# Performance work log

Measured on AMD Instinct MI355X. Metric: run time of the kernel, lower is better.

Reference implementation:

```python
import jax, jax.numpy as jnp
import numpy as np
from jax import lax


def conv2d_same(x, w):
    # x: [N,C,H,W], w: [O,I,3,3] -> [N,O,H,W], stride 1, padding 1
    return lax.conv_general_dilated(x, w, (1, 1), 'SAME',
                                    dimension_numbers=('NCHW', 'OIHW', 'NCHW'))


def bilinear_gather(x, py, px):
    # x: [N,C,H,W]; py,px: [N,K,H,W] float sampling coords (zero pad outside)
    # returns [N,C,K,H,W]
    N, C, H, W = x.shape
    y0f = jnp.floor(py)
    x0f = jnp.floor(px)
    wy = (py - y0f)[:, None]  # [N,1,K,H,W]
    wx = (px - x0f)[:, None]
    y0 = y0f.astype(jnp.int32)
    x0 = x0f.astype(jnp.int32)
    flat = x.reshape(N, C, H * W)

    def gather(yi, xi):
        valid = ((yi >= 0) & (yi < H) & (xi >= 0) & (xi < W))
        yc = jnp.clip(yi, 0, H - 1)
        xc = jnp.clip(xi, 0, W - 1)
        idx = (yc * W + xc).reshape(N, 1, -1)          # [N,1,K*H*W]
        g = jnp.take_along_axis(flat, jnp.broadcast_to(idx, (N, C, idx.shape[-1])), axis=2)
        g = g.reshape(N, C, *yi.shape[1:])             # [N,C,K,H,W]
        return g * valid.astype(x.dtype)[:, None]

    v00 = gather(y0, x0)
    v01 = gather(y0, x0 + 1)
    v10 = gather(y0 + 1, x0)
    v11 = gather(y0 + 1, x0 + 1)
    return (v00 * (1 - wy) * (1 - wx) + v01 * (1 - wy) * wx
            + v10 * wy * (1 - wx) + v11 * wy * wx)


def deform_conv(x, off, w, b):
    # x: [N,C,H,W]; off: [N,18,H,W] (dy,dx per 3x3 tap); w: [O,C,3,3]; b: [O]
    N, C, H, W = x.shape
    K = 9
    off = off.reshape(N, K, 2, H, W)
    kdy, kdx = jnp.meshgrid(jnp.arange(3) - 1, jnp.arange(3) - 1, indexing='ij')
    kdy = kdy.reshape(K).astype(x.dtype)
    kdx = kdx.reshape(K).astype(x.dtype)
    hh = jnp.arange(H, dtype=x.dtype)
    ww = jnp.arange(W, dtype=x.dtype)
    py = off[:, :, 0] + hh[None, None, :, None] + kdy[None, :, None, None]  # [N,K,H,W]
    px = off[:, :, 1] + ww[None, None, None, :] + kdx[None, :, None, None]
    sampled = bilinear_gather(x, py, px)               # [N,C,K,H,W]
    out = jnp.einsum('nckhw,ock->nohw', sampled, w.reshape(w.shape[0], C, K))
    return out + b[None, :, None, None]


def setup_inputs() -> dict:
    key = jax.random.key(0)
    ks = jax.random.split(key, 8)
    B, obj, C, H, W = 2, 4, 256, 48, 48
    return {
        'query': jax.random.normal(ks[0], (B, C, H, W), jnp.float32),
        'key': jax.random.normal(ks[1], (B, C, H, W), jnp.float32),
        'value': jax.random.normal(ks[2], (B, obj, C, H, W), jnp.float32),
        'off_conv_w': jax.random.normal(ks[3], (C, 2 * C, 3, 3), jnp.float32) * 0.02,
        'off_conv_b': jnp.zeros((C,), jnp.float32),
        'offp_w': jax.random.normal(ks[4], (18, C, 3, 3), jnp.float32) * 0.02,
        'offp_b': jnp.zeros((18,), jnp.float32),
        'deform_w': jax.random.normal(ks[5], (C, C, 3, 3), jnp.float32) * 0.02,
        'deform_b': jnp.zeros((C,), jnp.float32),
    }


def reference(query, key, value, off_conv_w, off_conv_b, offp_w, offp_b, deform_w, deform_b):
    B, obj, C, H, W = value.shape
    N = B * obj
    concat = jnp.concatenate([query, key], axis=1)                    # [B,2C,H,W]
    feat = conv2d_same(concat, off_conv_w) + off_conv_b[None, :, None, None]
    feat = jnp.broadcast_to(feat[:, None], (B, obj, C, H, W)).reshape(N, C, H, W)
    x = value.reshape(N, C, H, W)
    off = conv2d_same(feat, offp_w) + offp_b[None, :, None, None]     # [N,18,H,W]
    out = deform_conv(x, off, deform_w, deform_b)                     # [N,C,H,W]
    out = out.reshape(N, C, H * W).transpose(2, 0, 1)                 # [HW,N,C]
    q = jnp.broadcast_to(query[:, None], (B, obj, C, H, W)).reshape(N, C, H * W)
    return q.transpose(2, 0, 1) + out
```

## Files before the change

kernel.cpp:

```cpp
#include <hip/hip_runtime.h>

#define HH 48
#define WW 48
#define HWP 2304
#define CC 256
#define NB 8
#define QKROW 2305

typedef __attribute__((ext_vector_type(8))) short short8;
typedef __attribute__((ext_vector_type(4))) short bf16x4;
typedef __attribute__((ext_vector_type(4))) float floatx4;

static __device__ __forceinline__ unsigned short f2bf(float f) {
    union { float f; unsigned u; } v; v.f = f;
    unsigned r = v.u + 0x7fffu + ((v.u >> 16) & 1u);
    return (unsigned short)(r >> 16);
}
static __device__ __forceinline__ float bf2f(short v) {
    union { unsigned u; float f; } x; x.u = ((unsigned)(unsigned short)v) << 16;
    return x.f;
}

__global__ __launch_bounds__(256) void k_tr(const float* __restrict__ q,
        const float* __restrict__ kk, const float* __restrict__ v,
        unsigned short* __restrict__ qkT, float* __restrict__ qT,
        unsigned short* __restrict__ vT) {
    __shared__ float T[64][65];
    const int pg = blockIdx.x, cg = blockIdx.y, z = blockIdx.z;
    const int tx = threadIdx.x & 63, ty = threadIdx.x >> 6;
    if (z < 4) {
        const int b = z >> 1, src = z & 1;
        const float* s = (src ? kk : q) + (size_t)b * CC * HWP;
#pragma unroll
        for (int i = 0; i < 16; i++) {
            int cl = ty * 16 + i;
            T[cl][tx] = s[(size_t)(cg * 64 + cl) * HWP + pg * 64 + tx];
        }
        __syncthreads();
#pragma unroll
        for (int i = 0; i < 16; i++) {
            int pxl = ty * 16 + i;
            float val = T[tx][pxl];
            qkT[((size_t)b * QKROW + pg * 64 + pxl) * 512 + src * 256 + cg * 64 + tx]
                = f2bf(val);
            if (src == 0)
                qT[((size_t)(pg * 64 + pxl) * 2 + b) * 256 + cg * 64 + tx] = val;
        }
    } else {
        const int n = z - 4;
        const float* s = v + (size_t)n * CC * HWP;
#pragma unroll
        for (int i = 0; i < 16; i++) {
            int cl = ty * 16 + i;
            T[cl][tx] = s[(size_t)(cg * 64 + cl) * HWP + pg * 64 + tx];
        }
        __syncthreads();
#pragma unroll
        for (int i = 0; i < 16; i++) {
            int pxl = ty * 16 + i;
            vT[((size_t)n * HWP + pg * 64 + pxl) * 256 + cg * 64 + tx] = f2bf(T[tx][pxl]);
        }
    }
}

__global__ __launch_bounds__(256) void k_prep_w(const float* __restrict__ w1,
        const float* __restrict__ dw, const float* __restrict__ w2,
        unsigned short* __restrict__ w1r, unsigned short* __restrict__ wdr,
        unsigned short* __restrict__ w2r, unsigned short* __restrict__ qkT,
        unsigned short* __restrict__ featb) {
    if (blockIdx.x == 7200) {
        int t = threadIdx.x;
#pragma unroll
        for (int b = 0; b < 2; b++) {
            qkT[((size_t)b * QKROW + HWP) * 512 + t] = 0;
            qkT[((size_t)b * QKROW + HWP) * 512 + 256 + t] = 0;
            featb[((size_t)b * QKROW + HWP) * 256 + t] = 0;
        }
        return;
    }
    int idx = blockIdx.x * 256 + threadIdx.x;
    if (idx < 1179648) {
        int j = idx & 7, l = (idx >> 3) & 63, mtg = (idx >> 9) & 15;
        int kk = (idx >> 13) & 15, tap = idx >> 17;
        int o = mtg * 16 + (l & 15);
        int c2 = kk * 32 + (l >> 4) * 8 + j;
        w1r[idx] = f2bf(w1[((size_t)o * 512 + c2) * 9 + tap]);
    } else if (idx < 1179648 + 589824) {
        int i2 = idx - 1179648;
        int j = i2 & 7, l = (i2 >> 3) & 63, mtg = (i2 >> 9) & 15;
        int kk = (i2 >> 13) & 7, tap = i2 >> 16;
        int o = mtg * 16 + (l & 15);
        int c = kk * 32 + (l >> 4) * 8 + j;
        wdr[i2] = f2bf(dw[((size_t)o * 256 + c) * 9 + tap]);
    } else {
        int i2 = idx - 1179648 - 589824;
        int j = i2 & 7, l = (i2 >> 3) & 63, mt = (i2 >> 9) & 1;
        int kk = (i2 >> 10) & 7, tap = i2 >> 13;
        int o = mt * 16 + (l & 15);
        int c = kk * 32 + (l >> 4) * 8 + j;
        w2r[i2] = (o < 18) ? f2bf(w2[((size_t)o * 256 + c) * 9 + tap]) : 0;
    }
}

__global__ __launch_bounds__(512, 4) void k_conv1(const unsigned short* __restrict__ qkT,
        const unsigned short* __restrict__ w1r, const float* __restrict__ b1,
        unsigned short* __restrict__ featb) {
    __shared__ __align__(16) unsigned short Bl[2][32 * 64 * 8];

    const int tid = threadIdx.x;
    const int pt = blockIdx.x;
    const int b  = blockIdx.y;
    const int oh = blockIdx.z;
    const int px0 = pt * 32;
    const int lane = tid & 63, wv = tid >> 6;
    const int lo = lane & 15, quad = lane >> 4;
    const int mtg = oh * 8 + wv;

    floatx4 acc[2];
    acc[0] = (floatx4)0.f; acc[1] = (floatx4)0.f;

    short8 R[4];
    auto stage_load = [&](int tap) {
        const int dy = tap / 3 - 1, dx = tap % 3 - 1;
#pragma unroll
        for (int k = 0; k < 4; k++) {
            int seg = tid + k * 512;
            int cl  = seg >> 6;
            int sl  = seg & 63;
            int px  = px0 + cl;
            int h = px / WW, w = px - (px / WW) * WW;
            bool val = (h + dy >= 0) && (h + dy < HH)
                       && (w + dx >= 0) && (w + dx < WW);
            int row = val ? (px + dy * WW + dx) : HWP;
            R[k] = *(const short8*)(qkT + ((size_t)b * QKROW + row) * 512 + sl * 8);
        }
    };

    stage_load(0);
    int buf = 0;

    for (int tap = 0; tap < 9; tap++) {
        unsigned short* sb = &Bl[buf][0];
#pragma unroll
        for (int k = 0; k < 4; k++) {
            int seg = tid + k * 512;
            int cl = seg >> 6, sl = seg & 63;
            int slw = sl ^ (cl & 7);
            *(short8*)(sb + ((size_t)cl * 64 + slw) * 8) = R[k];
        }
        __syncthreads();

        if (tap < 8) stage_load(tap + 1);

        const unsigned short* afr = w1r + (((size_t)tap * 16 * 16 + mtg) * 64 + lane) * 8;
#pragma unroll 4
        for (int ks = 0; ks < 16; ks++) {
            short8 a = *(const short8*)(afr + (size_t)ks * 16 * 512);
#pragma unroll
            for (int nt = 0; nt < 2; nt++) {
                int cl = nt * 16 + lo;
                int slot = (ks * 4 + quad) ^ (cl & 7);
                short8 bf = *(const short8*)(sb + ((size_t)cl * 64 + slot) * 8);
                acc[nt] = __builtin_amdgcn_mfma_f32_16x16x32_bf16(a, bf, acc[nt], 0, 0, 0);
            }
        }
        buf ^= 1;
    }

    const int o = mtg * 16 + quad * 4;
    const float b0 = b1[o], bb1 = b1[o + 1], bb2 = b1[o + 2], bb3 = b1[o + 3];
#pragma unroll
    for (int nt = 0; nt < 2; nt++) {
        int px = px0 + nt * 16 + lo;
        bf16x4 pk;
        pk[0] = (short)f2bf(acc[nt][0] + b0);
        pk[1] = (short)f2bf(acc[nt][1] + bb1);
        pk[2] = (short)f2bf(acc[nt][2] + bb2);
        pk[3] = (short)f2bf(acc[nt][3] + bb3);
        *(bf16x4*)(featb + ((size_t)b * QKROW + px) * 256 + o) = pk;
    }
}

__global__ __launch_bounds__(256) void k_conv2(const unsigned short* __restrict__ featb,
        const unsigned short* __restrict__ w2r, float* __restrict__ off9) {
    const int tid = threadIdx.x;
    const int pb = blockIdx.x;
    const int b  = blockIdx.y;
    const int tap = blockIdx.z;
    const int lane = tid & 63, wv = tid >> 6;
    const int lo = lane & 15, quad = lane >> 4;
    const int pp = pb * 64 + wv * 16 + lo;
    const int h = pp / WW, w = pp - (pp / WW) * WW;
    const int dy = tap / 3 - 1, dx = tap % 3 - 1;
    const bool val = (h + dy >= 0) && (h + dy < HH) && (w + dx >= 0) && (w + dx < WW);
    const int row = val ? (pp + dy * WW + dx) : HWP;

    const unsigned short* brow = featb + ((size_t)b * QKROW + row) * 256 + quad * 8;
    const unsigned short* afr = w2r + (((size_t)tap * 8 * 2) * 64 + lane) * 8;

    floatx4 acc[2];
    acc[0] = (floatx4)0.f; acc[1] = (floatx4)0.f;
#pragma unroll
    for (int ks = 0; ks < 8; ks++) {
        short8 bf = *(const short8*)(brow + ks * 32);
        const unsigned short* ak = afr + (size_t)ks * 2 * 512;
        short8 a0 = *(const short8*)(ak);
        short8 a1 = *(const short8*)(ak + 512);
        acc[0] = __builtin_amdgcn_mfma_f32_16x16x32_bf16(a0, bf, acc[0], 0, 0, 0);
        acc[1] = __builtin_amdgcn_mfma_f32_16x16x32_bf16(a1, bf, acc[1], 0, 0, 0);
    }

    float* dst = off9 + (((size_t)tap * 2 + b) * HWP + pp) * 32;
#pragma unroll
    for (int mt = 0; mt < 2; mt++) {
        int o = mt * 16 + quad * 4;
        *(floatx4*)(dst + o) = acc[mt];
    }
}

__global__ __launch_bounds__(256) void k_osum(const float* __restrict__ off9,
        const float* __restrict__ b2, float* __restrict__ off) {
    int i = blockIdx.x * 256 + threadIdx.x;
    int b = i / (18 * HWP);
    int r = i - b * 18 * HWP;
    int o = r / HWP, px = r - o * HWP;
    float s = b2[o];
#pragma unroll
    for (int t = 0; t < 9; t++)
        s += off9[(((size_t)t * 2 + b) * HWP + px) * 32 + o];
    off[i] = s;
}

__global__ __launch_bounds__(512, 2) void k_deform(const unsigned short* __restrict__ vT,
        const float* __restrict__ off, const unsigned short* __restrict__ wdr,
        const float* __restrict__ db, const float* __restrict__ qT,
        float* __restrict__ out) {
    __shared__ __align__(16) unsigned short Sl[2][80 * 256];

    const int tid = threadIdx.x;
    const int bid = blockIdx.x;
    const int c0 = (((bid & 7) << 5) + (bid >> 3)) * 72;
    const int lane = tid & 63, wv = tid >> 6;
    const int lo = lane & 15, quad = lane >> 4;
    const int colg = tid >> 5;
    const int slice = tid & 31;

    int u_pq[5];
    float u_m[5];
    const float* u_off[5];
    const unsigned short* u_vT[5];
#pragma unroll
    for (int u = 0; u < 5; u++) {
        int cl = colg + u * 16;
        int cg = min(c0 + cl, 18431);
        int pq = cg >> 3, n = cg & 7;
        u_pq[u] = pq;
        u_m[u]  = (cl < 72) ? 1.f : 0.f;
        u_off[u] = off + (size_t)(n >> 2) * 18 * HWP + pq;
        u_vT[u]  = vT + (size_t)n * HWP * 256 + slice * 8;
    }

    floatx4 acc[2][5];
#pragma unroll
    for (int mt = 0; mt < 2; mt++)
#pragma unroll
        for (int nt = 0; nt < 5; nt++) acc[mt][nt] = (floatx4)0.f;

    short8 P[5][4];
    float  cwt[5][4];
    float  ndy[5], ndx[5];

    auto prefetch_off = [&](int tap) {
#pragma unroll
        for (int u = 0; u < 5; u++) {
            ndy[u] = u_off[u][(2 * tap) * HWP];
            ndx[u] = u_off[u][(2 * tap + 1) * HWP];
        }
    };

    auto prefetch_body = [&](int tap) {
        const float kdy = (float)(tap / 3 - 1), kdx = (float)(tap % 3 - 1);
#pragma unroll
        for (int u = 0; u < 5; u++) {
            int pq = u_pq[u];
            int h = pq / WW, w = pq - (pq / WW) * WW;
            float py = ndy[u] + (float)h + kdy;
            float px = ndx[u] + (float)w + kdx;
            float y0f = floorf(py), x0f = floorf(px);
            int y0 = (int)y0f, x0 = (int)x0f;
            float fy = py - y0f, fx = px - x0f;
            bool y0ok = (y0 >= 0) & (y0 < HH), y1ok = (y0 >= -1) & (y0 < HH - 1);
            bool x0ok = (x0 >= 0) & (x0 < WW), x1ok = (x0 >= -1) & (x0 < WW - 1);
            int y0c = min(max(y0, 0), HH - 1), y1c = min(max(y0 + 1, 0), HH - 1);
            int x0c = min(max(x0, 0), WW - 1), x1c = min(max(x0 + 1, 0), WW - 1);
            const unsigned short* r0 = u_vT[u] + (size_t)(y0c * WW + x0c) * 256;
            const unsigned short* r1 = u_vT[u] + (size_t)(y0c * WW + x1c) * 256;
            const unsigned short* r2 = u_vT[u] + (size_t)(y1c * WW + x0c) * 256;
            const unsigned short* r3 = u_vT[u] + (size_t)(y1c * WW + x1c) * 256;
            float m = u_m[u];
            cwt[u][0] = (y0ok && x0ok) ? m * (1.f - fy) * (1.f - fx) : 0.f;
            cwt[u][1] = (y0ok && x1ok) ? m * (1.f - fy) * fx         : 0.f;
            cwt[u][2] = (y1ok && x0ok) ? m * fy * (1.f - fx)         : 0.f;
            cwt[u][3] = (y1ok && x1ok) ? m * fy * fx                 : 0.f;
            P[u][0] = *(const short8*)(r0);
            P[u][1] = *(const short8*)(r1);
            P[u][2] = *(const short8*)(r2);
            P[u][3] = *(const short8*)(r3);
        }
    };

    prefetch_off(0);
    prefetch_body(0);
    int buf = 0;

    for (int tap = 0; tap < 9; tap++) {
        if (tap < 8) prefetch_off(tap + 1);
        unsigned short* sb = &Sl[buf][0];
#pragma unroll
        for (int u = 0; u < 5; u++) {
            float w0 = cwt[u][0], w1 = cwt[u][1], w2 = cwt[u][2], w3 = cwt[u][3];
            short8 ov;
#pragma unroll
            for (int j = 0; j < 8; j++) {
                float s = w0 * bf2f(P[u][0][j]) + w1 * bf2f(P[u][1][j])
                        + w2 * bf2f(P[u][2][j]) + w3 * bf2f(P[u][3][j]);
                ov[j] = (short)f2bf(s);
            }
            int cl = colg + u * 16;
            int slot = slice ^ (cl & 7);
            *(short8*)(sb + cl * 256 + slot * 8) = ov;
        }
        __syncthreads();

        if (tap < 8) prefetch_body(tap + 1);

        const unsigned short* afr = wdr + (((size_t)tap * 8 * 16 + wv * 2) * 64 + lane) * 8;
#pragma unroll
        for (int ks = 0; ks < 8; ks++) {
            const unsigned short* ak = afr + (size_t)ks * 16 * 512;
            short8 a0 = *(const short8*)(ak);
            short8 a1 = *(const short8*)(ak + 512);
#pragma unroll
            for (int nt = 0; nt < 5; nt++) {
                int cl = nt * 16 + lo;
                int slot = (ks * 4 + quad) ^ (cl & 7);
                short8 bf = *(const short8*)(sb + cl * 256 + slot * 8);
                acc[0][nt] = __builtin_amdgcn_mfma_f32_16x16x32_bf16(a0, bf, acc[0][nt], 0, 0, 0);
                acc[1][nt] = __builtin_amdgcn_mfma_f32_16x16x32_bf16(a1, bf, acc[1][nt], 0, 0, 0);
            }
        }
        __syncthreads();
        buf ^= 1;
    }

#pragma unroll
    for (int mt = 0; mt < 2; mt++) {
        int o = wv * 32 + mt * 16 + quad * 4;
        float d0 = db[o], d1 = db[o + 1], d2 = db[o + 2], d3 = db[o + 3];
#pragma unroll
        for (int nt = 0; nt < 5; nt++) {
            int cl = nt * 16 + lo;
            if (cl < 72) {
                int cg = c0 + cl;
                int pq = cg >> 3, b = (cg & 7) >> 2;
                floatx4 qv = *(const floatx4*)(qT + ((size_t)pq * 2 + b) * 256 + o);
                floatx4 r = acc[mt][nt];
                r[0] += d0 + qv[0];
                r[1] += d1 + qv[1];
                r[2] += d2 + qv[2];
                r[3] += d3 + qv[3];
                *(floatx4*)(out + (size_t)cg * CC + o) = r;
            }
        }
    }
}

extern "C" void kernel_launch(void* const* d_in, const int* in_sizes, int n_in,
                              void* d_out, int out_size, void* d_ws, size_t ws_size,
                              hipStream_t stream) {
    const float* q  = (const float*)d_in[0];
    const float* k  = (const float*)d_in[1];
    const float* v  = (const float*)d_in[2];
    const float* w1 = (const float*)d_in[3];
    const float* b1 = (const float*)d_in[4];
    const float* w2 = (const float*)d_in[5];
    const float* b2 = (const float*)d_in[6];
    const float* dw = (const float*)d_in[7];
    const float* db = (const float*)d_in[8];
    float* out = (float*)d_out;

    float* off   = (float*)d_ws;
    float* qT    = off + 82944;
    float* off9  = qT + 3538944;
    unsigned short* qkT   = (unsigned short*)(off9 + 1327104);
    unsigned short* vT    = qkT + 2360320;
    unsigned short* featb = vT + 4718592;
    unsigned short* w1r   = featb + 1180160;
    unsigned short* wdr   = w1r + 1179648;
    unsigned short* w2r   = wdr + 589824;

    hipLaunchKernelGGL(k_tr,    dim3(36, 4, 12), dim3(256), 0, stream, q, k, v, qkT, qT, vT);
    hipLaunchKernelGGL(k_prep_w,dim3(7201),      dim3(256), 0, stream, w1, dw, w2, w1r, wdr, w2r, qkT, featb);
    hipLaunchKernelGGL(k_conv1, dim3(72, 2, 2),  dim3(512), 0, stream, qkT, w1r, b1, featb);
    hipLaunchKernelGGL(k_conv2, dim3(36, 2, 9),  dim3(256), 0, stream, featb, w2r, off9);
    hipLaunchKernelGGL(k_osum,  dim3(324),       dim3(256), 0, stream, off9, b2, off);
    hipLaunchKernelGGL(k_deform,dim3(256),       dim3(512), 0, stream, vT, off, wdr, db, qT, out);
}
```

Measured before the change: 207.3 us.

## Merge transpose and weight-prep kernels; fuse tap reduction into offset conv

Combines the input transpose and weight reorder kernels into one launch with a flattened block index. Rewrites the offset conv so each block loops over all nine taps, staging shifted feature rows through double-buffered, swizzled shared memory and accumulating in registers. It then adds the bias and writes final offsets directly, removing the per-tap partial buffer and the separate summation kernel. This saves two launches and the partial-sum memory round-trip, but the conv now runs only 72 blocks, which reduces parallelism.

```diff
diff --git a/kernel.cpp b/kernel.cpp
--- a/kernel.cpp
+++ b/kernel.cpp
@@ -21,12 +21,54 @@
     return x.f;
 }
 
-__global__ __launch_bounds__(256) void k_tr(const float* __restrict__ q,
+__global__ __launch_bounds__(256) void k_trprep(const float* __restrict__ q,
         const float* __restrict__ kk, const float* __restrict__ v,
-        unsigned short* __restrict__ qkT, float* __restrict__ qT,
-        unsigned short* __restrict__ vT) {
+        const float* __restrict__ w1, const float* __restrict__ dw,
+        const float* __restrict__ w2, unsigned short* __restrict__ qkT,
+        float* __restrict__ qT, unsigned short* __restrict__ vT,
+        unsigned short* __restrict__ w1r, unsigned short* __restrict__ wdr,
+        unsigned short* __restrict__ w2r, unsigned short* __restrict__ featb) {
     __shared__ float T[64][65];
-    const int pg = blockIdx.x, cg = blockIdx.y, z = blockIdx.z;
+    const int bid = blockIdx.x;
+    if (bid < 7201) {
+        if (bid == 7200) {
+            int t = threadIdx.x;
+#pragma unroll
+            for (int b = 0; b < 2; b++) {
+                qkT[((size_t)b * QKROW + HWP) * 512 + t] = 0;
+                qkT[((size_t)b * QKROW + HWP) * 512 + 256 + t] = 0;
+                featb[((size_t)b * QKROW + HWP) * 256 + t] = 0;
+            }
+            return;
+        }
+        int idx = bid * 256 + threadIdx.x;
+        if (idx < 1179648) {
+            int j = idx & 7, l = (idx >> 3) & 63, mtg = (idx >> 9) & 15;
+            int kkk = (idx >> 13) & 15, tap = idx >> 17;
+            int o = mtg * 16 + (l & 15);
+            int c2 = kkk * 32 + (l >> 4) * 8 + j;
+            w1r[idx] = f2bf(w1[((size_t)o * 512 + c2) * 9 + tap]);
+        } else if (idx < 1179648 + 589824) {
+            int i2 = idx - 1179648;
+            int j = i2 & 7, l = (i2 >> 3) & 63, mtg = (i2 >> 9) & 15;
+            int kkk = (i2 >> 13) & 7, tap = i2 >> 16;
+            int o = mtg * 16 + (l & 15);
+            int c = kkk * 32 + (l >> 4) * 8 + j;
+            wdr[i2] = f2bf(dw[((size_t)o * 256 + c) * 9 + tap]);
+        } else {
+            int i2 = idx - 1179648 - 589824;
+            int j = i2 & 7, l = (i2 >> 3) & 63, mt = (i2 >> 9) & 1;
+            int kkk = (i2 >> 10) & 7, tap = i2 >> 13;
+            int o = mt * 16 + (l & 15);
+            int c = kkk * 32 + (l >> 4) * 8 + j;
+            w2r[i2] = (o < 18) ? f2bf(w2[((size_t)o * 256 + c) * 9 + tap]) : 0;
+        }
+        return;
+    }
+    const int idx2 = bid - 7201;
+    const int pg = idx2 % 36;
+    const int rest = idx2 / 36;
+    const int cg = rest & 3, z = rest >> 2;
     const int tx = threadIdx.x & 63, ty = threadIdx.x >> 6;
     if (z < 4) {
         const int b = z >> 1, src = z & 1;
@@ -60,45 +102,6 @@
             int pxl = ty * 16 + i;
             vT[((size_t)n * HWP + pg * 64 + pxl) * 256 + cg * 64 + tx] = f2bf(T[tx][pxl]);
         }
-    }
-}
-
-__global__ __launch_bounds__(256) void k_prep_w(const float* __restrict__ w1,
-        const float* __restrict__ dw, const float* __restrict__ w2,
-        unsigned short* __restrict__ w1r, unsigned short* __restrict__ wdr,
-        unsigned short* __restrict__ w2r, unsigned short* __restrict__ qkT,
-        unsigned short* __restrict__ featb) {
-    if (blockIdx.x == 7200) {
-        int t = threadIdx.x;
-#pragma unroll
-        for (int b = 0; b < 2; b++) {
-            qkT[((size_t)b * QKROW + HWP) * 512 + t] = 0;
-            qkT[((size_t)b * QKROW + HWP) * 512 + 256 + t] = 0;
-            featb[((size_t)b * QKROW + HWP) * 256 + t] = 0;
-        }
-        return;
-    }
-    int idx = blockIdx.x * 256 + threadIdx.x;
-    if (idx < 1179648) {
-        int j = idx & 7, l = (idx >> 3) & 63, mtg = (idx >> 9) & 15;
-        int kk = (idx >> 13) & 15, tap = idx >> 17;
-        int o = mtg * 16 + (l & 15);
-        int c2 = kk * 32 + (l >> 4) * 8 + j;
-        w1r[idx] = f2bf(w1[((size_t)o * 512 + c2) * 9 + tap]);
-    } else if (idx < 1179648 + 589824) {
-        int i2 = idx - 1179648;
-        int j = i2 & 7, l = (i2 >> 3) & 63, mtg = (i2 >> 9) & 15;
-        int kk = (i2 >> 13) & 7, tap = i2 >> 16;
-        int o = mtg * 16 + (l & 15);
-        int c = kk * 32 + (l >> 4) * 8 + j;
-        wdr[i2] = f2bf(dw[((size_t)o * 256 + c) * 9 + tap]);
-    } else {
-        int i2 = idx - 1179648 - 589824;
-        int j = i2 & 7, l = (i2 >> 3) & 63, mt = (i2 >> 9) & 1;
-        int kk = (i2 >> 10) & 7, tap = i2 >> 13;
-        int o = mt * 16 + (l & 15);
-        int c = kk * 32 + (l >> 4) * 8 + j;
-        w2r[i2] = (o < 18) ? f2bf(w2[((size_t)o * 256 + c) * 9 + tap]) : 0;
     }
 }
 
@@ -181,54 +184,74 @@
     }
 }
 
-__global__ __launch_bounds__(256) void k_conv2(const unsigned short* __restrict__ featb,
-        const unsigned short* __restrict__ w2r, float* __restrict__ off9) {
+__global__ __launch_bounds__(512, 2) void k_conv2(const unsigned short* __restrict__ featb,
+        const unsigned short* __restrict__ w2r, const float* __restrict__ b2,
+        float* __restrict__ off) {
+    __shared__ __align__(16) unsigned short Bl[2][64 * 32 * 8];
+
     const int tid = threadIdx.x;
-    const int pb = blockIdx.x;
+    const int pt = blockIdx.x;
     const int b  = blockIdx.y;
-    const int tap = blockIdx.z;
+    const int px0 = pt * 64;
     const int lane = tid & 63, wv = tid >> 6;
     const int lo = lane & 15, quad = lane >> 4;
-    const int pp = pb * 64 + wv * 16 + lo;
-    const int h = pp / WW, w = pp - (pp / WW) * WW;
-    const int dy = tap / 3 - 1, dx = tap % 3 - 1;
-    const bool val = (h + dy >= 0) && (h + dy < HH) && (w + dx >= 0) && (w + dx < WW);
-    const int row = val ? (pp + dy * WW + dx) : HWP;
-
-    const unsigned short* brow = featb + ((size_t)b * QKROW + row) * 256 + quad * 8;
-    const unsigned short* afr = w2r + (((size_t)tap * 8 * 2) * 64 + lane) * 8;
-
-    floatx4 acc[2];
-    acc[0] = (floatx4)0.f; acc[1] = (floatx4)0.f;
-#pragma unroll
-    for (int ks = 0; ks < 8; ks++) {
-        short8 bf = *(const short8*)(brow + ks * 32);
-        const unsigned short* ak = afr + (size_t)ks * 2 * 512;
-        short8 a0 = *(const short8*)(ak);
-        short8 a1 = *(const short8*)(ak + 512);
-        acc[0] = __builtin_amdgcn_mfma_f32_16x16x32_bf16(a0, bf, acc[0], 0, 0, 0);
-        acc[1] = __builtin_amdgcn_mfma_f32_16x16x32_bf16(a1, bf, acc[1], 0, 0, 0);
-    }
-
-    float* dst = off9 + (((size_t)tap * 2 + b) * HWP + pp) * 32;
-#pragma unroll
-    for (int mt = 0; mt < 2; mt++) {
-        int o = mt * 16 + quad * 4;
-        *(floatx4*)(dst + o) = acc[mt];
-    }
-}
-
-__global__ __launch_bounds__(256) void k_osum(const float* __restrict__ off9,
-        const float* __restrict__ b2, float* __restrict__ off) {
-    int i = blockIdx.x * 256 + threadIdx.x;
-    int b = i / (18 * HWP);
-    int r = i - b * 18 * HWP;
-    int o = r / HWP, px = r - o * HWP;
-    float s = b2[o];
-#pragma unroll
-    for (int t = 0; t < 9; t++)
-        s += off9[(((size_t)t * 2 + b) * HWP + px) * 32 + o];
-    off[i] = s;
+    const int mtg = wv & 1;
+    const int pxb = wv >> 1;
+
+    floatx4 acc = (floatx4)0.f;
+
+    short8 R[4];
+    auto stage_load = [&](int tap) {
+        const int dy = tap / 3 - 1, dx = tap % 3 - 1;
+#pragma unroll
+        for (int k = 0; k < 4; k++) {
+            int seg = tid + k * 512;
+            int cl  = seg >> 5;
+            int sl  = seg & 31;
+            int px  = px0 + cl;
+            int h = px / WW, w = px - (px / WW) * WW;
+            bool val = (h + dy >= 0) && (h + dy < HH)
+                       && (w + dx >= 0) && (w + dx < WW);
+            int row = val ? (px + dy * WW + dx) : HWP;
+            R[k] = *(const short8*)(featb + ((size_t)b * QKROW + row) * 256 + sl * 8);
+        }
+    };
+
+    stage_load(0);
+    int buf = 0;
+
+    for (int tap = 0; tap < 9; tap++) {
+        unsigned short* sb = &Bl[buf][0];
+#pragma unroll
+        for (int k = 0; k < 4; k++) {
+            int seg = tid + k * 512;
+            int cl = seg >> 5, sl = seg & 31;
+            int slw = sl ^ (cl & 7);
+            *(short8*)(sb + ((size_t)cl * 32 + slw) * 8) = R[k];
+        }
+        __syncthreads();
+
+        if (tap < 8) stage_load(tap + 1);
+
+#pragma unroll
+        for (int ks = 0; ks < 8; ks++) {
+            short8 a = *(const short8*)(w2r + ((((size_t)tap * 8 + ks) * 2 + mtg) * 64 + lane) * 8);
+            int cl = pxb * 16 + lo;
+            int slot = (ks * 4 + quad) ^ (cl & 7);
+            short8 bf = *(const short8*)(sb + ((size_t)cl * 32 + slot) * 8);
+            acc = __builtin_amdgcn_mfma_f32_16x16x32_bf16(a, bf, acc, 0, 0, 0);
+        }
+        buf ^= 1;
+    }
+
+    const int o = mtg * 16 + quad * 4;
+    const int px = px0 + pxb * 16 + lo;
+#pragma unroll
+    for (int i = 0; i < 4; i++) {
+        int oc = o + i;
+        if (oc < 18)
+            off[((size_t)b * 18 + oc) * HWP + px] = acc[i] + b2[oc];
+    }
 }
 
 __global__ __launch_bounds__(512, 2) void k_deform(const unsigned short* __restrict__ vT,
@@ -399,10 +422,9 @@
     unsigned short* wdr   = w1r + 1179648;
     unsigned short* w2r   = wdr + 589824;
 
-    hipLaunchKernelGGL(k_tr,    dim3(36, 4, 12), dim3(256), 0, stream, q, k, v, qkT, qT, vT);
-    hipLaunchKernelGGL(k_prep_w,dim3(7201),      dim3(256), 0, stream, w1, dw, w2, w1r, wdr, w2r, qkT, featb);
+    hipLaunchKernelGGL(k_trprep,dim3(8929),      dim3(256), 0, stream,
+                       q, k, v, w1, dw, w2, qkT, qT, vT, w1r, wdr, w2r, featb);
     hipLaunchKernelGGL(k_conv1, dim3(72, 2, 2),  dim3(512), 0, stream, qkT, w1r, b1, featb);
-    hipLaunchKernelGGL(k_conv2, dim3(36, 2, 9),  dim3(256), 0, stream, featb, w2r, off9);
-    hipLaunchKernelGGL(k_osum,  dim3(324),       dim3(256), 0, stream, off9, b2, off);
+    hipLaunchKernelGGL(k_conv2, dim3(36, 2),     dim3(512), 0, stream, featb, w2r, b2, off);
     hipLaunchKernelGGL(k_deform,dim3(256),       dim3(512), 0, stream, vT, off, wdr, db, qT, out);
 }
```

After: 205.1 us. No clear change (-1.1%).
